# Kernel tuning notes

Measured on AMD Instinct MI355X. Metric: run time of the kernel, lower is better.

The kernel has to match this reference:

```python
import jax, jax.numpy as jnp
import numpy as np


def setup_inputs() -> dict:
    key = jax.random.key(0)
    k1, k2, k3, k4 = jax.random.split(key, 4)
    Na, Nb, Da, Db, S = 200000, 200000, 64, 64, 256
    a_locations = jax.random.randint(k1, (Na, 3), 0, S, dtype=jnp.int32)
    b_locations = jax.random.randint(k2, (Nb, 3), 0, S, dtype=jnp.int32)
    a_features = jax.random.normal(k3, (Na, Da), dtype=jnp.float32)
    b_features = jax.random.normal(k4, (Nb, Db), dtype=jnp.float32)
    return {
        "a_locations": a_locations,
        "a_features": a_features,
        "b_locations": b_locations,
        "b_features": b_features,
    }


def reference(a_locations, a_features, b_locations, b_features):
    # Stack all locations and dedup rows (torch.unique(dim=0, return_inverse=True)).
    # For jit-compatibility we use size=N (worst case: no duplicates) and pad
    # trailing unused rows with fill_value=-1 (features rows stay zero).
    locations = jnp.concatenate([a_locations, b_locations], axis=0)  # [N, 3]
    N = locations.shape[0]
    unique_locations, reverse_indices = jnp.unique(
        locations, axis=0, size=N, fill_value=-1, return_inverse=True
    )
    reverse_indices = reverse_indices.ravel()  # [N]

    Na, Da = a_features.shape
    Db = b_features.shape[1]
    a_rev = reverse_indices[:Na]
    b_rev = reverse_indices[Na:]

    # Scatter-concat: a goes into columns [:Da], b into columns [Da:].
    unique_features = jnp.zeros((N, Da + Db), dtype=a_features.dtype)
    unique_features = unique_features.at[a_rev, :Da].set(a_features)
    unique_features = unique_features.at[b_rev, Da:].set(b_features)
    return unique_locations, unique_features
```

## Files before the change

### kernel.cpp

```cpp
#include <hip/hip_runtime.h>
#include <hip/hip_bf16.h>

#define NKEYS   (1 << 24)
#define NW      (NKEYS / 32)
#define WPT     4
#define TPB     256
#define WPB     (TPB * WPT)
#define NBLK2   (NW / WPB)
#define MAXN    400000

__device__ unsigned int g_bits[NW];
__device__ unsigned int g_wordPrefix[NW];
__device__ unsigned int g_blockSums[NBLK2];
__device__ int          g_winner_a[MAXN];
__device__ int          g_winner_b[MAXN];

__global__ void k_init(float* out_loc, int N) {
    int i = blockIdx.x * blockDim.x + threadIdx.x;
    if (i < NW / 4) reinterpret_cast<uint4*>(g_bits)[i] = make_uint4(0u, 0u, 0u, 0u);
    if (i < N) { g_winner_a[i] = -1; g_winner_b[i] = -1; }
    if (i < N * 3) out_loc[i] = -1.0f;
}

__global__ void k_mark(const int* __restrict__ a_loc, const int* __restrict__ b_loc,
                       int Na, int N) {
    int i = blockIdx.x * blockDim.x + threadIdx.x;
    if (i >= N) return;
    const int* p = (i < Na) ? (a_loc + (size_t)i * 3) : (b_loc + (size_t)(i - Na) * 3);
    int key = (p[0] << 16) | (p[1] << 8) | p[2];
    atomicOr(&g_bits[key >> 5], 1u << (key & 31));
}

__global__ void k_reduce() {
    __shared__ unsigned int s[TPB];
    int b = blockIdx.x, t = threadIdx.x;
    uint4 w = reinterpret_cast<const uint4*>(g_bits)[b * TPB + t];
    s[t] = __popc(w.x) + __popc(w.y) + __popc(w.z) + __popc(w.w);
    __syncthreads();
    for (int off = TPB / 2; off > 0; off >>= 1) {
        if (t < off) s[t] += s[t + off];
        __syncthreads();
    }
    if (t == 0) g_blockSums[b] = s[0];
}

__global__ void k_scan() {
    __shared__ unsigned int s[NBLK2];
    int t = threadIdx.x;
    unsigned int v = g_blockSums[t];
    s[t] = v;
    __syncthreads();
    for (int off = 1; off < NBLK2; off <<= 1) {
        unsigned int u = (t >= off) ? s[t - off] : 0u;
        __syncthreads();
        s[t] += u;
        __syncthreads();
    }
    g_blockSums[t] = s[t] - v;
}

__global__ void k_prefix_loc(float* __restrict__ out_loc) {
    __shared__ unsigned int s[TPB];
    int b = blockIdx.x, t = threadIdx.x;
    int w0 = (b * TPB + t) * WPT;
    uint4 wv = reinterpret_cast<const uint4*>(g_bits)[b * TPB + t];
    unsigned int wlocal[WPT] = { wv.x, wv.y, wv.z, wv.w };
    unsigned int cnt = __popc(wv.x) + __popc(wv.y) + __popc(wv.z) + __popc(wv.w);
    s[t] = cnt;
    __syncthreads();
    for (int off = 1; off < TPB; off <<= 1) {
        unsigned int u = (t >= off) ? s[t - off] : 0u;
        __syncthreads();
        s[t] += u;
        __syncthreads();
    }
    unsigned int r = g_blockSums[b] + s[t] - cnt;
#pragma unroll
    for (int j = 0; j < WPT; ++j) {
        unsigned int bits = wlocal[j];
        g_wordPrefix[w0 + j] = r;
        while (bits) {
            int bit = __ffs(bits) - 1;
            bits &= bits - 1;
            int key = ((w0 + j) << 5) | bit;
            float* p = out_loc + (size_t)r * 3;
            p[0] = (float)(key >> 16);
            p[1] = (float)((key >> 8) & 255);
            p[2] = (float)(key & 255);
            ++r;
        }
    }
}

__global__ void k_reverse(const int* __restrict__ a_loc, const int* __restrict__ b_loc,
                          int Na, int N) {
    int i = blockIdx.x * blockDim.x + threadIdx.x;
    if (i >= N) return;
    const int* p = (i < Na) ? (a_loc + (size_t)i * 3) : (b_loc + (size_t)(i - Na) * 3);
    int key = (p[0] << 16) | (p[1] << 8) | p[2];
    unsigned int word = g_bits[key >> 5];
    unsigned int r = g_wordPrefix[key >> 5] + __popc(word & ((1u << (key & 31)) - 1u));
    if (i < Na) atomicMax(&g_winner_a[r], i);
    else        atomicMax(&g_winner_b[r], i - Na);
}

__global__ void k_gather(const float* __restrict__ a_feat, const float* __restrict__ b_feat,
                         float* __restrict__ out_feat, int N) {
    int idx = blockIdx.x * blockDim.x + threadIdx.x;
    if (idx >= N * 32) return;
    int u  = idx >> 5;
    int c4 = (idx & 31) * 4;
    float4 v = make_float4(0.f, 0.f, 0.f, 0.f);
    if (c4 < 64) {
        int w = g_winner_a[u];
        if (w >= 0) v = *reinterpret_cast<const float4*>(a_feat + (size_t)w * 64 + c4);
    } else {
        int w = g_winner_b[u];
        if (w >= 0) v = *reinterpret_cast<const float4*>(b_feat + (size_t)w * 64 + (c4 - 64));
    }
    *reinterpret_cast<float4*>(out_feat + (size_t)u * 128 + c4) = v;
}

extern "C" void kernel_launch(void* const* d_in, const int* in_sizes, int n_in,
                              void* d_out, int out_size, void* d_ws, size_t ws_size,
                              hipStream_t stream) {
    const int*   a_loc  = (const int*)  d_in[0];
    const float* a_feat = (const float*)d_in[1];
    const int*   b_loc  = (const int*)  d_in[2];
    const float* b_feat = (const float*)d_in[3];

    const int Na = in_sizes[0] / 3;
    const int Nb = in_sizes[2] / 3;
    const int N  = Na + Nb;

    float* out_loc  = (float*)d_out;
    float* out_feat = out_loc + (size_t)N * 3;

    k_init<<<(N * 3 + TPB - 1) / TPB, TPB, 0, stream>>>(out_loc, N);
    k_mark<<<(N + TPB - 1) / TPB, TPB, 0, stream>>>(a_loc, b_loc, Na, N);
    k_reduce<<<NBLK2, TPB, 0, stream>>>();
    k_scan<<<1, NBLK2, 0, stream>>>();
    k_prefix_loc<<<NBLK2, TPB, 0, stream>>>(out_loc);
    k_reverse<<<(N + TPB - 1) / TPB, TPB, 0, stream>>>(a_loc, b_loc, Na, N);
    k_gather<<<(N * 32 + TPB - 1) / TPB, TPB, 0, stream>>>(a_feat, b_feat, out_feat, N);
}
```

Measured before the change: 153.6 us.

## Vectorize mark/reverse loads, fuse reduce+scan, nontemporal gather loads/stores

Mark and reverse kernels now process four points per thread using three 16-byte loads instead of scalar loads. The block-sum reduction and the single-block scan are fused into one kernel, where the last block to finish (tracked by an atomic counter) performs the scan, removing one launch. The gather kernel switches to nontemporal loads and stores so the streaming feature traffic bypasses cache retention. A scalar fallback path covers sizes not divisible by four.

```diff
diff --git a/kernel.cpp b/kernel.cpp
--- a/kernel.cpp
+++ b/kernel.cpp
@@ -3,68 +3,88 @@
 
 #define NKEYS   (1 << 24)
 #define NW      (NKEYS / 32)
-#define WPT     4
 #define TPB     256
-#define WPB     (TPB * WPT)
-#define NBLK2   (NW / WPB)
+#define NBLK    512
 #define MAXN    400000
+
+typedef float        f32x4 __attribute__((ext_vector_type(4)));
+typedef unsigned int u32x4 __attribute__((ext_vector_type(4)));
 
 __device__ unsigned int g_bits[NW];
 __device__ unsigned int g_wordPrefix[NW];
-__device__ unsigned int g_blockSums[NBLK2];
+__device__ unsigned int g_blockSums[NBLK];
+__device__ unsigned int g_doneCounter;
 __device__ int          g_winner_a[MAXN];
 __device__ int          g_winner_b[MAXN];
 
 __global__ void k_init(float* out_loc, int N) {
     int i = blockIdx.x * blockDim.x + threadIdx.x;
-    if (i < NW / 4) reinterpret_cast<uint4*>(g_bits)[i] = make_uint4(0u, 0u, 0u, 0u);
+    if (i < NW / 4) reinterpret_cast<u32x4*>(g_bits)[i] = (u32x4)(0u);
     if (i < N) { g_winner_a[i] = -1; g_winner_b[i] = -1; }
     if (i < N * 3) out_loc[i] = -1.0f;
-}
-
-__global__ void k_mark(const int* __restrict__ a_loc, const int* __restrict__ b_loc,
-                       int Na, int N) {
-    int i = blockIdx.x * blockDim.x + threadIdx.x;
-    if (i >= N) return;
-    const int* p = (i < Na) ? (a_loc + (size_t)i * 3) : (b_loc + (size_t)(i - Na) * 3);
-    int key = (p[0] << 16) | (p[1] << 8) | p[2];
-    atomicOr(&g_bits[key >> 5], 1u << (key & 31));
-}
-
-__global__ void k_reduce() {
+    if (i == 0) g_doneCounter = 0u;
+}
+
+__global__ void k_mark4(const int* __restrict__ a_loc, const int* __restrict__ b_loc,
+                        int nA4, int n4) {
+    int j = blockIdx.x * blockDim.x + threadIdx.x;
+    if (j >= n4) return;
+    const uint4* src = (j < nA4) ? reinterpret_cast<const uint4*>(a_loc)
+                                 : reinterpret_cast<const uint4*>(b_loc);
+    int jj = (j < nA4) ? j : j - nA4;
+    uint4 q0 = src[jj * 3], q1 = src[jj * 3 + 1], q2 = src[jj * 3 + 2];
+    int k0 = (q0.x << 16) | (q0.y << 8) | q0.z;
+    int k1 = (q0.w << 16) | (q1.x << 8) | q1.y;
+    int k2 = (q1.z << 16) | (q1.w << 8) | q2.x;
+    int k3 = (q2.y << 16) | (q2.z << 8) | q2.w;
+    atomicOr(&g_bits[k0 >> 5], 1u << (k0 & 31));
+    atomicOr(&g_bits[k1 >> 5], 1u << (k1 & 31));
+    atomicOr(&g_bits[k2 >> 5], 1u << (k2 & 31));
+    atomicOr(&g_bits[k3 >> 5], 1u << (k3 & 31));
+}
+
+__global__ void k_reduce_scan() {
     __shared__ unsigned int s[TPB];
+    __shared__ unsigned int isLast;
     int b = blockIdx.x, t = threadIdx.x;
-    uint4 w = reinterpret_cast<const uint4*>(g_bits)[b * TPB + t];
+    u32x4 w = reinterpret_cast<const u32x4*>(g_bits)[b * TPB + t];
     s[t] = __popc(w.x) + __popc(w.y) + __popc(w.z) + __popc(w.w);
     __syncthreads();
     for (int off = TPB / 2; off > 0; off >>= 1) {
         if (t < off) s[t] += s[t + off];
         __syncthreads();
     }
-    if (t == 0) g_blockSums[b] = s[0];
-}
-
-__global__ void k_scan() {
-    __shared__ unsigned int s[NBLK2];
-    int t = threadIdx.x;
-    unsigned int v = g_blockSums[t];
-    s[t] = v;
+    if (t == 0) {
+        g_blockSums[b] = s[0];
+        __threadfence();
+        unsigned int done = atomicAdd(&g_doneCounter, 1u);
+        isLast = (done == NBLK - 1) ? 1u : 0u;
+    }
     __syncthreads();
-    for (int off = 1; off < NBLK2; off <<= 1) {
-        unsigned int u = (t >= off) ? s[t - off] : 0u;
-        __syncthreads();
-        s[t] += u;
-        __syncthreads();
-    }
-    g_blockSums[t] = s[t] - v;
+    if (isLast) {
+        __threadfence();
+        unsigned int v0 = g_blockSums[t * 2], v1 = g_blockSums[t * 2 + 1];
+        unsigned int pair = v0 + v1;
+        s[t] = pair;
+        __syncthreads();
+        for (int off = 1; off < TPB; off <<= 1) {
+            unsigned int u = (t >= off) ? s[t - off] : 0u;
+            __syncthreads();
+            s[t] += u;
+            __syncthreads();
+        }
+        unsigned int excl = s[t] - pair;
+        g_blockSums[t * 2]     = excl;
+        g_blockSums[t * 2 + 1] = excl + v0;
+    }
 }
 
 __global__ void k_prefix_loc(float* __restrict__ out_loc) {
     __shared__ unsigned int s[TPB];
     int b = blockIdx.x, t = threadIdx.x;
-    int w0 = (b * TPB + t) * WPT;
-    uint4 wv = reinterpret_cast<const uint4*>(g_bits)[b * TPB + t];
-    unsigned int wlocal[WPT] = { wv.x, wv.y, wv.z, wv.w };
+    int w0 = (b * TPB + t) * 4;
+    u32x4 wv = reinterpret_cast<const u32x4*>(g_bits)[b * TPB + t];
+    unsigned int wlocal[4] = { wv.x, wv.y, wv.z, wv.w };
     unsigned int cnt = __popc(wv.x) + __popc(wv.y) + __popc(wv.z) + __popc(wv.w);
     s[t] = cnt;
     __syncthreads();
@@ -76,7 +96,7 @@
     }
     unsigned int r = g_blockSums[b] + s[t] - cnt;
 #pragma unroll
-    for (int j = 0; j < WPT; ++j) {
+    for (int j = 0; j < 4; ++j) {
         unsigned int bits = wlocal[j];
         g_wordPrefix[w0 + j] = r;
         while (bits) {
@@ -92,8 +112,41 @@
     }
 }
 
-__global__ void k_reverse(const int* __restrict__ a_loc, const int* __restrict__ b_loc,
-                          int Na, int N) {
+__global__ void k_reverse4(const int* __restrict__ a_loc, const int* __restrict__ b_loc,
+                           int nA4, int n4) {
+    int j = blockIdx.x * blockDim.x + threadIdx.x;
+    if (j >= n4) return;
+    bool isA = (j < nA4);
+    const uint4* src = isA ? reinterpret_cast<const uint4*>(a_loc)
+                           : reinterpret_cast<const uint4*>(b_loc);
+    int jj = isA ? j : j - nA4;
+    uint4 q0 = src[jj * 3], q1 = src[jj * 3 + 1], q2 = src[jj * 3 + 2];
+    int key[4];
+    key[0] = (q0.x << 16) | (q0.y << 8) | q0.z;
+    key[1] = (q0.w << 16) | (q1.x << 8) | q1.y;
+    key[2] = (q1.z << 16) | (q1.w << 8) | q2.x;
+    key[3] = (q2.y << 16) | (q2.z << 8) | q2.w;
+    int* winner = isA ? g_winner_a : g_winner_b;
+    int base = jj * 4;
+#pragma unroll
+    for (int k = 0; k < 4; ++k) {
+        int kk = key[k];
+        unsigned int word = g_bits[kk >> 5];
+        unsigned int r = g_wordPrefix[kk >> 5] + __popc(word & ((1u << (kk & 31)) - 1u));
+        atomicMax(&winner[r], base + k);
+    }
+}
+
+__global__ void k_mark1(const int* __restrict__ a_loc, const int* __restrict__ b_loc,
+                        int Na, int N) {
+    int i = blockIdx.x * blockDim.x + threadIdx.x;
+    if (i >= N) return;
+    const int* p = (i < Na) ? (a_loc + (size_t)i * 3) : (b_loc + (size_t)(i - Na) * 3);
+    int key = (p[0] << 16) | (p[1] << 8) | p[2];
+    atomicOr(&g_bits[key >> 5], 1u << (key & 31));
+}
+__global__ void k_reverse1(const int* __restrict__ a_loc, const int* __restrict__ b_loc,
+                           int Na, int N) {
     int i = blockIdx.x * blockDim.x + threadIdx.x;
     if (i >= N) return;
     const int* p = (i < Na) ? (a_loc + (size_t)i * 3) : (b_loc + (size_t)(i - Na) * 3);
@@ -110,15 +163,17 @@
     if (idx >= N * 32) return;
     int u  = idx >> 5;
     int c4 = (idx & 31) * 4;
-    float4 v = make_float4(0.f, 0.f, 0.f, 0.f);
+    f32x4 v = (f32x4)(0.f);
     if (c4 < 64) {
         int w = g_winner_a[u];
-        if (w >= 0) v = *reinterpret_cast<const float4*>(a_feat + (size_t)w * 64 + c4);
+        if (w >= 0) v = __builtin_nontemporal_load(
+                            reinterpret_cast<const f32x4*>(a_feat + (size_t)w * 64 + c4));
     } else {
         int w = g_winner_b[u];
-        if (w >= 0) v = *reinterpret_cast<const float4*>(b_feat + (size_t)w * 64 + (c4 - 64));
-    }
-    *reinterpret_cast<float4*>(out_feat + (size_t)u * 128 + c4) = v;
+        if (w >= 0) v = __builtin_nontemporal_load(
+                            reinterpret_cast<const f32x4*>(b_feat + (size_t)w * 64 + (c4 - 64)));
+    }
+    __builtin_nontemporal_store(v, reinterpret_cast<f32x4*>(out_feat + (size_t)u * 128 + c4));
 }
 
 extern "C" void kernel_launch(void* const* d_in, const int* in_sizes, int n_in,
@@ -137,10 +192,19 @@
     float* out_feat = out_loc + (size_t)N * 3;
 
     k_init<<<(N * 3 + TPB - 1) / TPB, TPB, 0, stream>>>(out_loc, N);
-    k_mark<<<(N + TPB - 1) / TPB, TPB, 0, stream>>>(a_loc, b_loc, Na, N);
-    k_reduce<<<NBLK2, TPB, 0, stream>>>();
-    k_scan<<<1, NBLK2, 0, stream>>>();
-    k_prefix_loc<<<NBLK2, TPB, 0, stream>>>(out_loc);
-    k_reverse<<<(N + TPB - 1) / TPB, TPB, 0, stream>>>(a_loc, b_loc, Na, N);
+
+    if ((Na % 4) == 0 && (Nb % 4) == 0) {
+        int nA4 = Na / 4, n4 = (Na + Nb) / 4;
+        k_mark4<<<(n4 + TPB - 1) / TPB, TPB, 0, stream>>>(a_loc, b_loc, nA4, n4);
+        k_reduce_scan<<<NBLK, TPB, 0, stream>>>();
+        k_prefix_loc<<<NBLK, TPB, 0, stream>>>(out_loc);
+        k_reverse4<<<(n4 + TPB - 1) / TPB, TPB, 0, stream>>>(a_loc, b_loc, nA4, n4);
+    } else {
+        k_mark1<<<(N + TPB - 1) / TPB, TPB, 0, stream>>>(a_loc, b_loc, Na, N);
+        k_reduce_scan<<<NBLK, TPB, 0, stream>>>();
+        k_prefix_loc<<<NBLK, TPB, 0, stream>>>(out_loc);
+        k_reverse1<<<(N + TPB - 1) / TPB, TPB, 0, stream>>>(a_loc, b_loc, Na, N);
+    }
+
     k_gather<<<(N * 32 + TPB - 1) / TPB, TPB, 0, stream>>>(a_feat, b_feat, out_feat, N);
 }
```

Result: no change. 153.1 us (-0.3%).
